# Optimization experiments

Measured on AMD Instinct MI355X. Metric: run time of the kernel, lower is better.

The kernel has to match this reference:

```python
import jax, jax.numpy as jnp
import numpy as np

# plan steps: (downsample_factor, bins_min, bins_max)
PLAN = [(2, 10, 14), (4, 16, 20)]


def _downsample(x, scale):
    # F.interpolate(mode='linear', align_corners=False, scale_factor=1/scale)
    in_len = x.shape[-1]
    out_len = in_len // scale
    sf = in_len / out_len
    src = jnp.maximum((jnp.arange(out_len, dtype=jnp.float32) + 0.5) * sf - 0.5, 0.0)
    i0 = jnp.floor(src).astype(jnp.int32)
    w = src - i0
    i1 = jnp.minimum(i0 + 1, in_len - 1)
    return x[..., i0] * (1.0 - w) + x[..., i1] * w


def _groupshiftadd(x, g):
    # one FFA butterfly stage with group size g
    B, C, R, nc = x.shape
    xg = x.reshape(B, C, R // g, g, nc)
    i = np.arange(g)
    iA = i // 2
    iB = iA + g // 2
    Bs = (i + 1) // 2
    # roll(v, Bs): y[j] = v[(j - Bs) mod nc]; static gather indices
    col = (np.arange(nc)[None, :] - Bs[:, None]) % nc  # (g, nc)
    a = xg[:, :, :, iA, :]                     # (B,C,G,g,nc)
    b = xg[:, :, :, iB[:, None], col]          # (B,C,G,g,nc) shifted rows
    return (a + b).reshape(B, C, R, nc)


def _forward(x):
    std_dev = jnp.std(x, axis=2, ddof=1)  # torch .std(2) is unbiased
    outs = []
    for ds, bmin, bmax in PLAN:
        down = _downsample(x, ds)
        L = down.shape[-1]
        for bins in range(bmin, bmax):
            trunc = L % bins
            arr = down[:, :, :L - trunc] if trunc else down
            r = arr.reshape(arr.shape[0], arr.shape[1], -1, bins)
            ini_rows = r.shape[2]
            k = int(np.ceil(np.log2(ini_rows)))
            target_rows = 2 ** k
            add = target_rows - ini_rows
            if add:
                pad = jnp.zeros((r.shape[0], r.shape[1], add, bins), r.dtype)
                r = jnp.concatenate([r, pad], axis=2)
            y = r
            for stage in range(1, k + 1):
                y = _groupshiftadd(y, 2 ** stage)
            mx = y.max(axis=3)
            # torch.median returns lower middle element for even sizes
            med = jnp.sort(y, axis=3)[..., (bins - 1) // 2]
            snr = (mx - med) / std_dev[:, :, None] / np.sqrt(float(ini_rows))
            outs.append(snr)  # (B, C, target_rows)
    return jnp.concatenate(outs, axis=2)


def setup_inputs() -> dict:
    key = jax.random.key(0)
    x = jax.random.normal(key, (8, 4, 262144), dtype=jnp.float32)
    return {"x": x}


def reference(x):
    return _forward(x)
```

## Files before the change

kernel.cpp:

```cpp
#include <hip/hip_runtime.h>
#include <cmath>


constexpr int NSEQ    = 32;
constexpr int NLEN    = 262144;
constexpr int OUTROWS = 81920;
constexpr int STDCH   = 32;

constexpr int cilog2(int v) { int r = 0; while (v > 1) { v >>= 1; ++r; } return r; }

constexpr size_t SCROFF[8] = {0, 6291456, 12582912, 18874368,
                              27262976, 29360128, 31981568, 34603008};

__device__ __forceinline__ unsigned bf16rne(float f) {
    unsigned u = __float_as_uint(f);
    return (u + 0x7FFFu + ((u >> 16) & 1u)) >> 16;
}
__device__ __forceinline__ unsigned pk2(float lo, float hi) {
    return bf16rne(lo) | (bf16rne(hi) << 16);
}
__device__ __forceinline__ int swz(int r) { return r ^ (((r >> 4) & 7) << 2); }

__device__ __forceinline__ void wfence()
{
    __builtin_amdgcn_sched_barrier(0);
    asm volatile("s_waitcnt lgkmcnt(0)" ::: "memory");
    __builtin_amdgcn_sched_barrier(0);
    __builtin_amdgcn_wave_barrier();
}

template<bool BAR>
__device__ __forceinline__ void stsync()
{
    if constexpr (BAR) __syncthreads();
    else wfence();
}

__global__ __launch_bounds__(256)
void std_partial(const float* __restrict__ x, float2* __restrict__ part)
{
    const int seq = blockIdx.x, ch = blockIdx.y;
    constexpr int N4 = NLEN / 4 / STDCH;
    const float4* xp = reinterpret_cast<const float4*>(x + (size_t)seq * NLEN) + (size_t)ch * N4;
    float s = 0.f, s2 = 0.f;
    for (int i = threadIdx.x; i < N4; i += 256) {
        float4 v = xp[i];
        s  += (v.x + v.y) + (v.z + v.w);
        s2 += (v.x * v.x + v.y * v.y) + (v.z * v.z + v.w * v.w);
    }
    #pragma unroll
    for (int off = 32; off > 0; off >>= 1) {
        s  += __shfl_down(s, off, 64);
        s2 += __shfl_down(s2, off, 64);
    }
    __shared__ float2 ws[4];
    const int w = threadIdx.x >> 6, l = threadIdx.x & 63;
    if (l == 0) ws[w] = make_float2(s, s2);
    __syncthreads();
    if (threadIdx.x == 0) {
        float a = ws[0].x + ws[1].x + ws[2].x + ws[3].x;
        float b = ws[0].y + ws[1].y + ws[2].y + ws[3].y;
        part[seq * STDCH + ch] = make_float2(a, b);
    }
}

template<int BINS, int G, int HB, bool BAR>
__device__ __forceinline__
void fusedA1ip(float* __restrict__ buf, int Q, int c0)
{
    constexpr int CST = G + 4;
    const int r4 = swz(4 * Q);
    float4 ff[HB + 3];
    #pragma unroll
    for (int j = 0; j < HB + 3; ++j) {
        int cc = c0 - 3 + j;
        if (cc < 0) cc += BINS;
        if (cc >= BINS) cc -= BINS;
        ff[j] = *reinterpret_cast<const float4*>(&buf[cc * CST + r4]);
    }
    stsync<BAR>();
    #pragma unroll
    for (int i = 0; i < HB; ++i) {
        const int c = c0 + i;
        if (c < BINS) {
            float4 f = ff[i + 3], fm1 = ff[i + 2], fm2 = ff[i + 1], fm3 = ff[i];
            float u0 = f.x + f.y;
            float u1 = f.x + fm1.y;
            float4 o;
            o.x = u0 + (f.z + f.w);
            o.y = u0 + (fm1.z + fm1.w);
            o.z = u1 + (fm1.z + fm2.w);
            o.w = u1 + (fm2.z + fm3.w);
            *reinterpret_cast<float4*>(&buf[c * CST + r4]) = o;
        }
    }
    stsync<BAR>();
}

template<int BINS, int G, int HB, bool BAR>
__device__ __forceinline__
void fusedAip(float* __restrict__ buf, int s, int Q, int c0)
{
    constexpr int CST = G + 4;
    const int h = 1 << (s - 1), S = 1 << s;
    const int q  = Q & (h - 1);
    const int G2 = (Q >> (s - 1)) << (s + 1);
    const int rA0 = swz(G2 + q),     rA1 = swz(G2 + q + h);
    const int rB0 = swz(G2 + S + q), rB1 = swz(G2 + S + q + h);
    const int vo  = swz(G2 + 4 * q);
    auto mbf = [](int x) { int r = x % BINS; return r < 0 ? r + BINS : r; };
    const int ba1 = mbf(c0 - q - 1);
    const int bb0 = mbf(c0 - 2 * q - 2);
    const int bb1 = mbf(c0 - 3 * q - 3);

    float fa0[HB], fa1[HB + 1], fb0[HB + 2], fb1[HB + 3];
    #pragma unroll
    for (int i = 0; i < HB; ++i) {
        int cc = c0 + i; if (cc >= BINS) cc = BINS - 1;
        fa0[i] = buf[cc * CST + rA0];
    }
    int idx = ba1;
    #pragma unroll
    for (int i = 0; i < HB + 1; ++i) {
        fa1[i] = buf[idx * CST + rA1];
        ++idx; if (idx == BINS) idx = 0;
    }
    idx = bb0;
    #pragma unroll
    for (int i = 0; i < HB + 2; ++i) {
        fb0[i] = buf[idx * CST + rB0];
        ++idx; if (idx == BINS) idx = 0;
    }
    idx = bb1;
    #pragma unroll
    for (int i = 0; i < HB + 3; ++i) {
        fb1[i] = buf[idx * CST + rB1];
        ++idx; if (idx == BINS) idx = 0;
    }
    stsync<BAR>();
    #pragma unroll
    for (int i = 0; i < HB; ++i) {
        const int c = c0 + i;
        if (c < BINS) {
            float u0 = fa0[i] + fa1[i + 1];
            float u1 = fa0[i] + fa1[i];
            float v0c  = fb0[i + 2] + fb1[i + 3];
            float v0p  = fb0[i + 1] + fb1[i + 2];
            float v1p  = fb0[i + 1] + fb1[i + 1];
            float v1pp = fb0[i]     + fb1[i];
            float4 o; o.x = u0 + v0c; o.y = u0 + v0p; o.z = u1 + v1p; o.w = u1 + v1pp;
            *reinterpret_cast<float4*>(&buf[c * CST + vo]) = o;
        }
    }
    stsync<BAR>();
}

template<int BINS, int G, int H1>
__device__ __forceinline__
void stage9IP(float* __restrict__ buf, int pr, int c0)
{
    constexpr int CST = G + 4;
    const int sA = swz(pr);
    const int sB = sA + 256;
    const int so = swz(2 * pr);
    const int shift = pr % BINS;

    float ra[H1], rb[H1 + 1];
    #pragma unroll
    for (int i = 0; i < H1; ++i) {
        int cc = c0 + i; if (cc >= BINS) cc = BINS - 1;
        ra[i] = buf[cc * CST + sA];
    }
    int idx = c0 - shift - 1;
    idx %= BINS; if (idx < 0) idx += BINS;
    #pragma unroll
    for (int i = 0; i < H1 + 1; ++i) {
        rb[i] = buf[idx * CST + sB];
        ++idx; if (idx == BINS) idx = 0;
    }
    __syncthreads();
    #pragma unroll
    for (int i = 0; i < H1; ++i) {
        const int c = c0 + i;
        if (c < BINS) {
            float2 o; o.x = ra[i] + rb[i + 1]; o.y = ra[i] + rb[i];
            *reinterpret_cast<float2*>(&buf[c * CST + so]) = o;
        }
    }
    __syncthreads();
}

template<int DS, int BINS, int K, int S0, int CPAD>
__device__ __forceinline__
void passA_body(float* __restrict__ buf, const float* __restrict__ xs,
                unsigned short* __restrict__ scrC, int R, int blk, int sl)
{
    constexpr int G     = 1 << S0;
    constexpr int M     = 1 << (K - S0);
    constexpr int CST   = G + 4;
    constexpr int QUADS = G / 4;
    constexpr int CHB   = 512 / QUADS;
    constexpr int LCHB  = cilog2(CHB);
    constexpr int QPW   = QUADS / 8;
    constexpr int HB    = (BINS + CHB - 1) / CHB;
    constexpr int CS1   = 512 / (G / 2);
    constexpr int H1    = (BINS + CS1 - 1) / CS1;
    const int t = threadIdx.x;

    const int fmax = max(0, min(G * BINS, R * BINS - blk * G * BINS));
    if (fmax <= 0) return;

    if constexpr (DS == 2) {
        const float4* src4 = reinterpret_cast<const float4*>(xs + 2 * (size_t)blk * G * BINS);
        constexpr int NF4 = G * BINS / 2;
        for (int i = t; i < NF4; i += 512) {
            const int f0 = 2 * i;
            if (f0 < fmax) {
                float4 v = src4[i];
                int lr = f0 / BINS, c = f0 - lr * BINS;
                buf[c * CST + swz(lr)] = 0.5f * (v.x + v.y);
                if (f0 + 1 < fmax) {
                    int c1 = c + 1, lr1 = lr;
                    if (c1 == BINS) { c1 = 0; ++lr1; }
                    buf[c1 * CST + swz(lr1)] = 0.5f * (v.z + v.w);
                }
            }
        }
    } else {
        const float4* src4 = reinterpret_cast<const float4*>(xs + 4 * (size_t)blk * G * BINS);
        constexpr int NF4 = G * BINS;
        for (int i = t; i < NF4; i += 512) {
            if (i < fmax) {
                float4 v = src4[i];
                int lr = i / BINS, c = i - lr * BINS;
                buf[c * CST + swz(lr)] = 0.5f * (v.y + v.z);
            }
        }
    }
    for (int f = fmax + t; f < G * BINS; f += 512) {
        int lr = f / BINS, c = f - lr * BINS;
        buf[c * CST + swz(lr)] = 0.f;
    }
    __syncthreads();

    {
        const int w = t >> 6, l = t & 63;
        const int Q  = w * QPW + (l >> LCHB);
        const int c0 = (l & (CHB - 1)) * HB;
        if constexpr (S0 == 9) {
            fusedA1ip<BINS, G, HB, false>(buf, Q, c0);
            fusedAip <BINS, G, HB, false>(buf, 3, Q, c0);
            fusedAip <BINS, G, HB, false>(buf, 5, Q, c0);
            __syncthreads();
            fusedAip <BINS, G, HB, true >(buf, 7, Q, c0);
        } else {
            fusedA1ip<BINS, G, HB, false>(buf, Q, c0);
            fusedAip <BINS, G, HB, false>(buf, 3, Q, c0);
            __syncthreads();
            fusedAip <BINS, G, HB, true >(buf, 5, Q, c0);
            fusedAip <BINS, G, HB, true >(buf, 7, Q, c0);
        }
    }
    if constexpr (S0 == 9) {
        const int pr  = t & (G / 2 - 1);
        const int c01 = (t >> (S0 - 1)) * H1;
        stage9IP<BINS, G, H1>(buf, pr, c01);
    }

    const float* fin = buf;
    if constexpr (G == 512) {
        const int lr = swz(t);
        unsigned u[CPAD / 2];
        #pragma unroll
        for (int k = 0; k < CPAD / 2; ++k) {
            const int ca = 2 * k, cbn = 2 * k + 1;
            float fa = (ca < BINS)  ? fin[ca * CST + lr]  : 0.f;
            float fb = (cbn < BINS) ? fin[cbn * CST + lr] : 0.f;
            u[k] = pk2(fa, fb);
        }
        unsigned short* dst = scrC + ((size_t)(sl * M + blk) * G + t) * CPAD;
        if constexpr (CPAD == 12) {
            uint2* d2 = reinterpret_cast<uint2*>(dst);
            d2[0] = make_uint2(u[0], u[1]);
            d2[1] = make_uint2(u[2], u[3]);
            d2[2] = make_uint2(u[4], u[5]);
        } else {
            uint4* d4 = reinterpret_cast<uint4*>(dst);
            d4[0] = make_uint4(u[0], u[1], u[2], u[3]);
            d4[1] = make_uint4(u[4], u[5], u[6], u[7]);
        }
    } else {
        const int lrn = t & 255, chh = t >> 8;
        const int lr = swz(lrn);
        constexpr int CH = CPAD / 2;
        unsigned u[CH / 2];
        #pragma unroll
        for (int k = 0; k < CH / 2; ++k) {
            const int ca = chh * CH + 2 * k, cbn = ca + 1;
            float fa = (ca < BINS)  ? fin[ca * CST + lr]  : 0.f;
            float fb = (cbn < BINS) ? fin[cbn * CST + lr] : 0.f;
            u[k] = pk2(fa, fb);
        }
        unsigned short* dst = scrC + ((size_t)(sl * M + blk) * G + lrn) * CPAD + chh * CH;
        if constexpr (CH == 8) {
            *reinterpret_cast<uint4*>(dst) = make_uint4(u[0], u[1], u[2], u[3]);
        } else {
            unsigned* d = reinterpret_cast<unsigned*>(dst);
            #pragma unroll
            for (int k = 0; k < CH / 2; ++k) d[k] = u[k];
        }
    }
}

__global__ __launch_bounds__(512, 6)
void passA_all(const float* __restrict__ x, unsigned short* __restrict__ scr)
{
    __shared__ float buf[13 * 516];
    const int b = blockIdx.x;
    if (b < 4096) {
        const int cfg = b >> 10, r = b & 1023, blk = r & 31, sl = r >> 5;
        const float* xs = x + (size_t)sl * NLEN;
        switch (cfg) {
            case 0: passA_body<2, 10, 14, 9, 12>(buf, xs, scr + SCROFF[0], 13107, blk, sl); break;
            case 1: passA_body<2, 11, 14, 9, 12>(buf, xs, scr + SCROFF[1], 11915, blk, sl); break;
            case 2: passA_body<2, 12, 14, 9, 12>(buf, xs, scr + SCROFF[2], 10922, blk, sl); break;
            default: passA_body<2, 13, 14, 9, 16>(buf, xs, scr + SCROFF[3], 10082, blk, sl); break;
        }
    } else {
        const int b2 = b - 4096;
        const int cfg = b2 >> 9, r = b2 & 511, blk = r & 15, sl = r >> 4;
        const float* xs = x + (size_t)sl * NLEN;
        switch (cfg) {
            case 0: passA_body<4, 16, 12, 8, 16>(buf, xs, scr + SCROFF[4], 4096, blk, sl); break;
            case 1: passA_body<4, 17, 12, 8, 20>(buf, xs, scr + SCROFF[5], 3855, blk, sl); break;
            case 2: passA_body<4, 18, 12, 8, 20>(buf, xs, scr + SCROFF[6], 3640, blk, sl); break;
            default: passA_body<4, 19, 12, 8, 20>(buf, xs, scr + SCROFF[7], 3449, blk, sl); break;
        }
    }
}

template<int BINS, int M, int CST, int HB, int LQ>
__device__ __forceinline__
void fusedB(float* __restrict__ zpg, int s, int p, int sub)
{
    constexpr int QUADS = M / 4;
    const int Q   = sub & (QUADS - 1);
    const int chi = sub >> LQ;
    const int c0  = chi * HB;
    const int h = 1 << (s - 1), S = 1 << s;
    const int q  = Q & (h - 1);
    const int G2 = (Q >> (s - 1)) << (s + 1);
    const int rA0 = G2 + q, rA1 = rA0 + h, rB0 = G2 + S + q, rB1 = rB0 + h;
    const int vo = G2 + 4 * q;
    auto mbf = [](int x, int B) { int r = x % B; return r < 0 ? r + B : r; };
    const int ba1 = mbf(c0 - q - p * h - 1, BINS);
    const int bb0 = mbf(c0 - 2 * q - p * S - 2, BINS);
    const int bb1 = mbf(c0 - 3 * q - p * (S + h) - 3, BINS);

    float fa0[HB], fa1[HB + 1], fb0[HB + 2], fb1[HB + 3];
    #pragma unroll
    for (int i = 0; i < HB; ++i) {
        int cc = c0 + i; if (cc >= BINS) cc = BINS - 1;
        fa0[i] = zpg[cc * CST + rA0];
    }
    int idx = ba1;
    #pragma unroll
    for (int i = 0; i < HB + 1; ++i) {
        fa1[i] = zpg[idx * CST + rA1];
        ++idx; if (idx == BINS) idx = 0;
    }
    idx = bb0;
    #pragma unroll
    for (int i = 0; i < HB + 2; ++i) {
        fb0[i] = zpg[idx * CST + rB0];
        ++idx; if (idx == BINS) idx = 0;
    }
    idx = bb1;
    #pragma unroll
    for (int i = 0; i < HB + 3; ++i) {
        fb1[i] = zpg[idx * CST + rB1];
        ++idx; if (idx == BINS) idx = 0;
    }
    __syncthreads();
    #pragma unroll
    for (int i2 = 0; i2 < HB; ++i2) {
        const int c = c0 + i2;
        if (c < BINS) {
            float u0 = fa0[i2] + fa1[i2 + 1];
            float u1 = fa0[i2] + fa1[i2];
            float v0c  = fb0[i2 + 2] + fb1[i2 + 3];
            float v0p  = fb0[i2 + 1] + fb1[i2 + 2];
            float v1p  = fb0[i2 + 1] + fb1[i2 + 1];
            float v1pp = fb0[i2]     + fb1[i2];
            float4 o; o.x = u0 + v0c; o.y = u0 + v0p; o.z = u1 + v1p; o.w = u1 + v1pp;
            *reinterpret_cast<float4*>(&zpg[c * CST + vo]) = o;
        }
    }
    __syncthreads();
}

template<int BINS, int M, int CST, int HSB, int LP>
__device__ __forceinline__
void singleB(float* __restrict__ zpg, int s, int p, int sub)
{
    constexpr int PAIRSB = M / 2;
    const int pr  = sub & (PAIRSB - 1);
    const int chi = sub >> LP;
    const int c0  = chi * HSB;
    const int half = 1 << (s - 1);
    const int qp = pr & (half - 1);
    const int grpbase = (pr >> (s - 1)) << s;
    const int rA = grpbase + qp, rB = rA + half, ro = grpbase + 2 * qp;
    const int shift = (qp + p * half) % BINS;

    float ra[HSB], rb[HSB + 1];
    #pragma unroll
    for (int i = 0; i < HSB; ++i) {
        int cc = c0 + i; if (cc >= BINS) cc = BINS - 1;
        ra[i] = zpg[cc * CST + rA];
    }
    int idx = c0 - shift - 1;
    idx %= BINS; if (idx < 0) idx += BINS;
    #pragma unroll
    for (int i = 0; i < HSB + 1; ++i) {
        rb[i] = zpg[idx * CST + rB];
        ++idx; if (idx == BINS) idx = 0;
    }
    __syncthreads();
    #pragma unroll
    for (int i2 = 0; i2 < HSB; ++i2) {
        const int c = c0 + i2;
        if (c < BINS) {
            float2 o; o.x = ra[i2] + rb[i2 + 1]; o.y = ra[i2] + rb[i2];
            *reinterpret_cast<float2*>(&zpg[c * CST + ro]) = o;
        }
    }
    __syncthreads();
}

template<int BINS, int K, int S0, int CPAD, int OUTOFF>
__device__ __forceinline__
void passB_body(float* __restrict__ zb, float* __restrict__ s_red,
                const unsigned short* __restrict__ scrC, const float2* __restrict__ part,
                float* __restrict__ out, int R, int p_base, int sl)
{
    constexpr int G    = 1 << S0;
    constexpr int M    = 1 << (K - S0);
    constexpr int TS   = K - S0;
    constexpr int P    = 16;
    constexpr int CST  = M + 4;
    constexpr int BCST = BINS * CST;
    constexpr int LQB  = cilog2(M / 4);
    constexpr int CHB  = 32 / (M / 4);
    constexpr int HB   = (BINS + CHB - 1) / CHB;
    constexpr int LPB  = cilog2(M / 2);
    constexpr int CSB  = 32 / (M / 2);
    constexpr int HSB  = (BINS + CSB - 1) / CSB;

    const int t = threadIdx.x;

    if (t < 64) {
        float s = 0.f, s2 = 0.f;
        if (t < 32) { float2 pp = part[sl * STDCH + t]; s = pp.x; s2 = pp.y; }
        #pragma unroll
        for (int off = 16; off > 0; off >>= 1) {
            s  += __shfl_down(s, off, 64);
            s2 += __shfl_down(s2, off, 64);
        }
        if (t == 0) {
            const float n = (float)NLEN;
            s_red[0] = rsqrtf((s2 - s * s / n) / (n - 1.f)) * rsqrtf((float)R);
        }
    }

    {
        constexpr int RUN = P * CPAD / 4;
        constexpr int TOT = M * RUN;
        const int vmax = (R + G - 1) >> S0;
        const unsigned short* base = scrC + (size_t)sl * M * G * CPAD + (size_t)p_base * CPAD;
        for (int i = t; i < TOT; i += 512) {
            const int v = i / RUN, r = i - v * RUN;
            uint2 d = make_uint2(0u, 0u);
            if (v < vmax)
                d = *reinterpret_cast<const uint2*>(base + (size_t)v * G * CPAD + 4 * r);
            const int e0 = 4 * r;
            const int pl = e0 / CPAD, c = e0 - pl * CPAD;
            float* zp = zb + pl * BCST + v;
            if (c + 0 < BINS) zp[(c + 0) * CST] = __uint_as_float(d.x << 16);
            if (c + 1 < BINS) zp[(c + 1) * CST] = __uint_as_float(d.x & 0xFFFF0000u);
            if (c + 2 < BINS) zp[(c + 2) * CST] = __uint_as_float(d.y << 16);
            if (c + 3 < BINS) zp[(c + 3) * CST] = __uint_as_float(d.y & 0xFFFF0000u);
        }
    }
    __syncthreads();

    const int sub = t & 31, pg = t >> 5;
    const int p = p_base + pg;
    float* zpg = zb + pg * BCST;
    fusedB<BINS, M, CST, HB, LQB>(zpg, 1, p, sub);
    fusedB<BINS, M, CST, HB, LQB>(zpg, 3, p, sub);
    if constexpr (TS == 5) {
        singleB<BINS, M, CST, HSB, LPB>(zpg, 5, p, sub);
    }

    constexpr int ROWS = P * M;
    if (t < ROWS) {
        const int pg2 = t >> TS;
        const int v   = t & (M - 1);
        const float* z = zb + pg2 * BCST;
        float a[BINS];
        #pragma unroll
        for (int c = 0; c < BINS; ++c) a[c] = z[c * CST + v];
        float mx = a[0];
        #pragma unroll
        for (int c = 1; c < BINS; ++c) mx = fmaxf(mx, a[c]);
        constexpr int MIDX = (BINS - 1) / 2;
        #pragma unroll
        for (int i = 0; i <= MIDX; ++i) {
            #pragma unroll
            for (int j = i + 1; j < BINS; ++j) {
                float lo = fminf(a[i], a[j]);
                float hi = fmaxf(a[i], a[j]);
                a[i] = lo; a[j] = hi;
            }
        }
        out[(size_t)sl * OUTROWS + OUTOFF + (size_t)p_base * M + t] = (mx - a[MIDX]) * s_red[0];
    }
}

__global__ __launch_bounds__(512, 6)
void passB_all(const unsigned short* __restrict__ scr, const float2* __restrict__ part,
               float* __restrict__ out)
{
    __shared__ float zb[16 * 13 * 36];
    __shared__ float s_red[1];
    const int b = blockIdx.x;
    if (b < 4096) {
        const int cfg = b >> 10, r = b & 1023, pb = r & 31, sl = r >> 5;
        const int p_base = pb * 16;
        switch (cfg) {
            case 0: passB_body<10, 14, 9, 12, 0>    (zb, s_red, scr + SCROFF[0], part, out, 13107, p_base, sl); break;
            case 1: passB_body<11, 14, 9, 12, 16384>(zb, s_red, scr + SCROFF[1], part, out, 11915, p_base, sl); break;
            case 2: passB_body<12, 14, 9, 12, 32768>(zb, s_red, scr + SCROFF[2], part, out, 10922, p_base, sl); break;
            default: passB_body<13, 14, 9, 16, 49152>(zb, s_red, scr + SCROFF[3], part, out, 10082, p_base, sl); break;
        }
    } else {
        const int b2 = b - 4096;
        const int cfg = b2 >> 9, r = b2 & 511, pb = r & 15, sl = r >> 4;
        const int p_base = pb * 16;
        switch (cfg) {
            case 0: passB_body<16, 12, 8, 16, 65536>(zb, s_red, scr + SCROFF[4], part, out, 4096, p_base, sl); break;
            case 1: passB_body<17, 12, 8, 20, 69632>(zb, s_red, scr + SCROFF[5], part, out, 3855, p_base, sl); break;
            case 2: passB_body<18, 12, 8, 20, 73728>(zb, s_red, scr + SCROFF[6], part, out, 3640, p_base, sl); break;
            default: passB_body<19, 12, 8, 20, 77824>(zb, s_red, scr + SCROFF[7], part, out, 3449, p_base, sl); break;
        }
    }
}

extern "C" void kernel_launch(void* const* d_in, const int* in_sizes, int n_in,
                              void* d_out, int out_size, void* d_ws, size_t ws_size,
                              hipStream_t stream)
{
    (void)in_sizes; (void)n_in; (void)out_size; (void)ws_size;
    const float* x = (const float*)d_in[0];
    float* out  = (float*)d_out;
    float* wsf  = (float*)d_ws;
    float2* part = reinterpret_cast<float2*>(wsf + 64);
    unsigned short* scr = reinterpret_cast<unsigned short*>(wsf + 2176);

    hipLaunchKernelGGL(std_partial, dim3(NSEQ, STDCH), dim3(256), 0, stream, x, part);
    hipLaunchKernelGGL(passA_all, dim3(6144), dim3(512), 0, stream, x, scr);
    hipLaunchKernelGGL(passB_all, dim3(6144), dim3(512), 0, stream, scr, part, out);
}
```

Measured before the change: 144.7 us.

## Split FFA stages as 8+6 for ds=2 configs, use 256-thread passA blocks

Pass A now always handles a 256-row group (8 butterfly stages) with 256-thread blocks, so the ds=2 configurations launch twice as many smaller blocks and no longer need the separate stage-9 in-place step with its extra barriers. Pass B in turn takes over the sixth stage for those configurations, processing 8 periods per block with 64 threads each and running three fused stage pairs. This trades a larger pass-B working set and different LDS footprints for smaller pass-A blocks, higher occupancy and fewer block-wide syncs.

Measured after the change: 142.2 us (median of 2 runs). Within noise of the previous version (-1.8%).

```diff
diff --git a/kernel.cpp b/kernel.cpp
--- a/kernel.cpp
+++ b/kernel.cpp
@@ -28,7 +28,6 @@
     __builtin_amdgcn_sched_barrier(0);
     __builtin_amdgcn_wave_barrier();
 }
-
 template<bool BAR>
 __device__ __forceinline__ void stsync()
 {
@@ -155,56 +154,20 @@
     stsync<BAR>();
 }
 
-template<int BINS, int G, int H1>
-__device__ __forceinline__
-void stage9IP(float* __restrict__ buf, int pr, int c0)
-{
-    constexpr int CST = G + 4;
-    const int sA = swz(pr);
-    const int sB = sA + 256;
-    const int so = swz(2 * pr);
-    const int shift = pr % BINS;
-
-    float ra[H1], rb[H1 + 1];
-    #pragma unroll
-    for (int i = 0; i < H1; ++i) {
-        int cc = c0 + i; if (cc >= BINS) cc = BINS - 1;
-        ra[i] = buf[cc * CST + sA];
-    }
-    int idx = c0 - shift - 1;
-    idx %= BINS; if (idx < 0) idx += BINS;
-    #pragma unroll
-    for (int i = 0; i < H1 + 1; ++i) {
-        rb[i] = buf[idx * CST + sB];
-        ++idx; if (idx == BINS) idx = 0;
-    }
-    __syncthreads();
-    #pragma unroll
-    for (int i = 0; i < H1; ++i) {
-        const int c = c0 + i;
-        if (c < BINS) {
-            float2 o; o.x = ra[i] + rb[i + 1]; o.y = ra[i] + rb[i];
-            *reinterpret_cast<float2*>(&buf[c * CST + so]) = o;
-        }
-    }
-    __syncthreads();
-}
-
-template<int DS, int BINS, int K, int S0, int CPAD>
+template<int DS, int BINS, int K, int CPAD>
 __device__ __forceinline__
 void passA_body(float* __restrict__ buf, const float* __restrict__ xs,
                 unsigned short* __restrict__ scrC, int R, int blk, int sl)
 {
-    constexpr int G     = 1 << S0;
+    constexpr int S0    = 8;
+    constexpr int G     = 256;
     constexpr int M     = 1 << (K - S0);
     constexpr int CST   = G + 4;
     constexpr int QUADS = G / 4;
-    constexpr int CHB   = 512 / QUADS;
-    constexpr int LCHB  = cilog2(CHB);
-    constexpr int QPW   = QUADS / 8;
+    constexpr int CHB   = 4;
+    constexpr int LCHB  = 2;
+    constexpr int QPW   = QUADS / 4;
     constexpr int HB    = (BINS + CHB - 1) / CHB;
-    constexpr int CS1   = 512 / (G / 2);
-    constexpr int H1    = (BINS + CS1 - 1) / CS1;
     const int t = threadIdx.x;
 
     const int fmax = max(0, min(G * BINS, R * BINS - blk * G * BINS));
@@ -213,7 +176,7 @@
     if constexpr (DS == 2) {
         const float4* src4 = reinterpret_cast<const float4*>(xs + 2 * (size_t)blk * G * BINS);
         constexpr int NF4 = G * BINS / 2;
-        for (int i = t; i < NF4; i += 512) {
+        for (int i = t; i < NF4; i += 256) {
             const int f0 = 2 * i;
             if (f0 < fmax) {
                 float4 v = src4[i];
@@ -229,7 +192,7 @@
     } else {
         const float4* src4 = reinterpret_cast<const float4*>(xs + 4 * (size_t)blk * G * BINS);
         constexpr int NF4 = G * BINS;
-        for (int i = t; i < NF4; i += 512) {
+        for (int i = t; i < NF4; i += 256) {
             if (i < fmax) {
                 float4 v = src4[i];
                 int lr = i / BINS, c = i - lr * BINS;
@@ -237,7 +200,7 @@
             }
         }
     }
-    for (int f = fmax + t; f < G * BINS; f += 512) {
+    for (int f = fmax + t; f < G * BINS; f += 256) {
         int lr = f / BINS, c = f - lr * BINS;
         buf[c * CST + swz(lr)] = 0.f;
     }
@@ -247,94 +210,60 @@
         const int w = t >> 6, l = t & 63;
         const int Q  = w * QPW + (l >> LCHB);
         const int c0 = (l & (CHB - 1)) * HB;
-        if constexpr (S0 == 9) {
-            fusedA1ip<BINS, G, HB, false>(buf, Q, c0);
-            fusedAip <BINS, G, HB, false>(buf, 3, Q, c0);
-            fusedAip <BINS, G, HB, false>(buf, 5, Q, c0);
-            __syncthreads();
-            fusedAip <BINS, G, HB, true >(buf, 7, Q, c0);
-        } else {
-            fusedA1ip<BINS, G, HB, false>(buf, Q, c0);
-            fusedAip <BINS, G, HB, false>(buf, 3, Q, c0);
-            __syncthreads();
-            fusedAip <BINS, G, HB, true >(buf, 5, Q, c0);
-            fusedAip <BINS, G, HB, true >(buf, 7, Q, c0);
-        }
-    }
-    if constexpr (S0 == 9) {
-        const int pr  = t & (G / 2 - 1);
-        const int c01 = (t >> (S0 - 1)) * H1;
-        stage9IP<BINS, G, H1>(buf, pr, c01);
-    }
-
-    const float* fin = buf;
-    if constexpr (G == 512) {
+        fusedA1ip<BINS, G, HB, false>(buf, Q, c0);
+        fusedAip <BINS, G, HB, false>(buf, 3, Q, c0);
+        fusedAip <BINS, G, HB, false>(buf, 5, Q, c0);
+        __syncthreads();
+        fusedAip <BINS, G, HB, true >(buf, 7, Q, c0);
+    }
+
+    {
         const int lr = swz(t);
         unsigned u[CPAD / 2];
         #pragma unroll
         for (int k = 0; k < CPAD / 2; ++k) {
             const int ca = 2 * k, cbn = 2 * k + 1;
-            float fa = (ca < BINS)  ? fin[ca * CST + lr]  : 0.f;
-            float fb = (cbn < BINS) ? fin[cbn * CST + lr] : 0.f;
+            float fa = (ca < BINS)  ? buf[ca * CST + lr]  : 0.f;
+            float fb = (cbn < BINS) ? buf[cbn * CST + lr] : 0.f;
             u[k] = pk2(fa, fb);
         }
         unsigned short* dst = scrC + ((size_t)(sl * M + blk) * G + t) * CPAD;
-        if constexpr (CPAD == 12) {
-            uint2* d2 = reinterpret_cast<uint2*>(dst);
-            d2[0] = make_uint2(u[0], u[1]);
-            d2[1] = make_uint2(u[2], u[3]);
-            d2[2] = make_uint2(u[4], u[5]);
-        } else {
+        if constexpr (CPAD == 16) {
             uint4* d4 = reinterpret_cast<uint4*>(dst);
             d4[0] = make_uint4(u[0], u[1], u[2], u[3]);
             d4[1] = make_uint4(u[4], u[5], u[6], u[7]);
-        }
-    } else {
-        const int lrn = t & 255, chh = t >> 8;
-        const int lr = swz(lrn);
-        constexpr int CH = CPAD / 2;
-        unsigned u[CH / 2];
-        #pragma unroll
-        for (int k = 0; k < CH / 2; ++k) {
-            const int ca = chh * CH + 2 * k, cbn = ca + 1;
-            float fa = (ca < BINS)  ? fin[ca * CST + lr]  : 0.f;
-            float fb = (cbn < BINS) ? fin[cbn * CST + lr] : 0.f;
-            u[k] = pk2(fa, fb);
-        }
-        unsigned short* dst = scrC + ((size_t)(sl * M + blk) * G + lrn) * CPAD + chh * CH;
-        if constexpr (CH == 8) {
-            *reinterpret_cast<uint4*>(dst) = make_uint4(u[0], u[1], u[2], u[3]);
         } else {
-            unsigned* d = reinterpret_cast<unsigned*>(dst);
+            uint2* d2 = reinterpret_cast<uint2*>(dst);
             #pragma unroll
-            for (int k = 0; k < CH / 2; ++k) d[k] = u[k];
-        }
-    }
-}
-
-__global__ __launch_bounds__(512, 6)
+            for (int k = 0; k < CPAD / 4; ++k)
+                d2[k] = make_uint2(u[2 * k], u[2 * k + 1]);
+        }
+    }
+}
+
+__global__ __launch_bounds__(256, 8)
 void passA_all(const float* __restrict__ x, unsigned short* __restrict__ scr)
 {
-    __shared__ float buf[13 * 516];
+    __shared__ float buf[19 * 260];
     const int b = blockIdx.x;
-    if (b < 4096) {
-        const int cfg = b >> 10, r = b & 1023, blk = r & 31, sl = r >> 5;
+    if (b < 8192) {
+        const int cfg = b >> 11, r = b & 2047, blk = r & 63, sl = r >> 6;
         const float* xs = x + (size_t)sl * NLEN;
         switch (cfg) {
-            case 0: passA_body<2, 10, 14, 9, 12>(buf, xs, scr + SCROFF[0], 13107, blk, sl); break;
-            case 1: passA_body<2, 11, 14, 9, 12>(buf, xs, scr + SCROFF[1], 11915, blk, sl); break;
-            case 2: passA_body<2, 12, 14, 9, 12>(buf, xs, scr + SCROFF[2], 10922, blk, sl); break;
-            default: passA_body<2, 13, 14, 9, 16>(buf, xs, scr + SCROFF[3], 10082, blk, sl); break;
+            case 0: passA_body<2, 10, 14, 12>(buf, xs, scr + SCROFF[0], 13107, blk, sl); break;
+            case 1: passA_body<2, 11, 14, 12>(buf, xs, scr + SCROFF[1], 11915, blk, sl); break;
+            case 2: passA_body<2, 12, 14, 12>(buf, xs, scr + SCROFF[2], 10922, blk, sl); break;
+            default: passA_body<2, 13, 14, 16>(buf, xs, scr + SCROFF[3], 10082, blk, sl); break;
         }
     } else {
-        const int b2 = b - 4096;
+        const int b2 = b - 8192;
         const int cfg = b2 >> 9, r = b2 & 511, blk = r & 15, sl = r >> 4;
         const float* xs = x + (size_t)sl * NLEN;
         switch (cfg) {
-            case 0: passA_body<4, 16, 12, 8, 16>(buf, xs, scr + SCROFF[4], 4096, blk, sl); break;
-            case 1: passA_body<4, 17, 12, 8, 20>(buf, xs, scr + SCROFF[5], 3855, blk, sl); break;
-            case 2: passA_body<4, 18, 12, 8, 20>(buf, xs, scr + SCROFF[6], 3640, blk, sl); break;
-            default: passA_body<4, 19, 12, 8, 20>(buf, xs, scr + SCROFF[7], 3449, blk, sl); break;
+            case 0: passA_body<4, 16, 12, 16>(buf, xs, scr + SCROFF[4], 4096, blk, sl); break;
+            case 1: passA_body<4, 17, 12, 20>(buf, xs, scr + SCROFF[5], 3855, blk, sl); break;
+            case 2: passA_body<4, 18, 12, 20>(buf, xs, scr + SCROFF[6], 3640, blk, sl); break;
+            default: passA_body<4, 19, 12, 20>(buf, xs, scr + SCROFF[7], 3449, blk, sl); break;
         }
     }
 }
@@ -399,63 +328,23 @@
     __syncthreads();
 }
 
-template<int BINS, int M, int CST, int HSB, int LP>
-__device__ __forceinline__
-void singleB(float* __restrict__ zpg, int s, int p, int sub)
-{
-    constexpr int PAIRSB = M / 2;
-    const int pr  = sub & (PAIRSB - 1);
-    const int chi = sub >> LP;
-    const int c0  = chi * HSB;
-    const int half = 1 << (s - 1);
-    const int qp = pr & (half - 1);
-    const int grpbase = (pr >> (s - 1)) << s;
-    const int rA = grpbase + qp, rB = rA + half, ro = grpbase + 2 * qp;
-    const int shift = (qp + p * half) % BINS;
-
-    float ra[HSB], rb[HSB + 1];
-    #pragma unroll
-    for (int i = 0; i < HSB; ++i) {
-        int cc = c0 + i; if (cc >= BINS) cc = BINS - 1;
-        ra[i] = zpg[cc * CST + rA];
-    }
-    int idx = c0 - shift - 1;
-    idx %= BINS; if (idx < 0) idx += BINS;
-    #pragma unroll
-    for (int i = 0; i < HSB + 1; ++i) {
-        rb[i] = zpg[idx * CST + rB];
-        ++idx; if (idx == BINS) idx = 0;
-    }
-    __syncthreads();
-    #pragma unroll
-    for (int i2 = 0; i2 < HSB; ++i2) {
-        const int c = c0 + i2;
-        if (c < BINS) {
-            float2 o; o.x = ra[i2] + rb[i2 + 1]; o.y = ra[i2] + rb[i2];
-            *reinterpret_cast<float2*>(&zpg[c * CST + ro]) = o;
-        }
-    }
-    __syncthreads();
-}
-
-template<int BINS, int K, int S0, int CPAD, int OUTOFF>
+template<int BINS, int K, int P, int CPAD, int OUTOFF>
 __device__ __forceinline__
 void passB_body(float* __restrict__ zb, float* __restrict__ s_red,
                 const unsigned short* __restrict__ scrC, const float2* __restrict__ part,
                 float* __restrict__ out, int R, int p_base, int sl)
 {
-    constexpr int G    = 1 << S0;
+    constexpr int S0   = 8;
+    constexpr int G    = 256;
     constexpr int M    = 1 << (K - S0);
     constexpr int TS   = K - S0;
-    constexpr int P    = 16;
     constexpr int CST  = M + 4;
     constexpr int BCST = BINS * CST;
+    constexpr int SUBW = 512 / P;
+    constexpr int LSUB = cilog2(SUBW);
     constexpr int LQB  = cilog2(M / 4);
-    constexpr int CHB  = 32 / (M / 4);
+    constexpr int CHB  = SUBW / (M / 4);
     constexpr int HB   = (BINS + CHB - 1) / CHB;
-    constexpr int LPB  = cilog2(M / 2);
-    constexpr int CSB  = 32 / (M / 2);
-    constexpr int HSB  = (BINS + CSB - 1) / CSB;
 
     const int t = threadIdx.x;
 
@@ -494,14 +383,12 @@
     }
     __syncthreads();
 
-    const int sub = t & 31, pg = t >> 5;
+    const int sub = t & (SUBW - 1), pg = t >> LSUB;
     const int p = p_base + pg;
     float* zpg = zb + pg * BCST;
-    fusedB<BINS, M, CST, HB, LQB>(zpg, 1, p, sub);
-    fusedB<BINS, M, CST, HB, LQB>(zpg, 3, p, sub);
-    if constexpr (TS == 5) {
-        singleB<BINS, M, CST, HSB, LPB>(zpg, 5, p, sub);
-    }
+    #pragma unroll
+    for (int s = 1; s <= TS; s += 2)
+        fusedB<BINS, M, CST, HB, LQB>(zpg, s, p, sub);
 
     constexpr int ROWS = P * M;
     if (t < ROWS) {
@@ -532,27 +419,27 @@
 void passB_all(const unsigned short* __restrict__ scr, const float2* __restrict__ part,
                float* __restrict__ out)
 {
-    __shared__ float zb[16 * 13 * 36];
+    __shared__ float zb[8 * 13 * 68];
     __shared__ float s_red[1];
     const int b = blockIdx.x;
     if (b < 4096) {
         const int cfg = b >> 10, r = b & 1023, pb = r & 31, sl = r >> 5;
-        const int p_base = pb * 16;
+        const int p_base = pb * 8;
         switch (cfg) {
-            case 0: passB_body<10, 14, 9, 12, 0>    (zb, s_red, scr + SCROFF[0], part, out, 13107, p_base, sl); break;
-            case 1: passB_body<11, 14, 9, 12, 16384>(zb, s_red, scr + SCROFF[1], part, out, 11915, p_base, sl); break;
-            case 2: passB_body<12, 14, 9, 12, 32768>(zb, s_red, scr + SCROFF[2], part, out, 10922, p_base, sl); break;
-            default: passB_body<13, 14, 9, 16, 49152>(zb, s_red, scr + SCROFF[3], part, out, 10082, p_base, sl); break;
+            case 0: passB_body<10, 14, 8, 12, 0>    (zb, s_red, scr + SCROFF[0], part, out, 13107, p_base, sl); break;
+            case 1: passB_body<11, 14, 8, 12, 16384>(zb, s_red, scr + SCROFF[1], part, out, 11915, p_base, sl); break;
+            case 2: passB_body<12, 14, 8, 12, 32768>(zb, s_red, scr + SCROFF[2], part, out, 10922, p_base, sl); break;
+            default: passB_body<13, 14, 8, 16, 49152>(zb, s_red, scr + SCROFF[3], part, out, 10082, p_base, sl); break;
         }
     } else {
         const int b2 = b - 4096;
         const int cfg = b2 >> 9, r = b2 & 511, pb = r & 15, sl = r >> 4;
         const int p_base = pb * 16;
         switch (cfg) {
-            case 0: passB_body<16, 12, 8, 16, 65536>(zb, s_red, scr + SCROFF[4], part, out, 4096, p_base, sl); break;
-            case 1: passB_body<17, 12, 8, 20, 69632>(zb, s_red, scr + SCROFF[5], part, out, 3855, p_base, sl); break;
-            case 2: passB_body<18, 12, 8, 20, 73728>(zb, s_red, scr + SCROFF[6], part, out, 3640, p_base, sl); break;
-            default: passB_body<19, 12, 8, 20, 77824>(zb, s_red, scr + SCROFF[7], part, out, 3449, p_base, sl); break;
+            case 0: passB_body<16, 12, 16, 16, 65536>(zb, s_red, scr + SCROFF[4], part, out, 4096, p_base, sl); break;
+            case 1: passB_body<17, 12, 16, 20, 69632>(zb, s_red, scr + SCROFF[5], part, out, 3855, p_base, sl); break;
+            case 2: passB_body<18, 12, 16, 20, 73728>(zb, s_red, scr + SCROFF[6], part, out, 3640, p_base, sl); break;
+            default: passB_body<19, 12, 16, 20, 77824>(zb, s_red, scr + SCROFF[7], part, out, 3449, p_base, sl); break;
         }
     }
 }
@@ -569,6 +456,6 @@
     unsigned short* scr = reinterpret_cast<unsigned short*>(wsf + 2176);
 
     hipLaunchKernelGGL(std_partial, dim3(NSEQ, STDCH), dim3(256), 0, stream, x, part);
-    hipLaunchKernelGGL(passA_all, dim3(6144), dim3(512), 0, stream, x, scr);
+    hipLaunchKernelGGL(passA_all, dim3(10240), dim3(256), 0, stream, x, scr);
     hipLaunchKernelGGL(passB_all, dim3(6144), dim3(512), 0, stream, scr, part, out);
 }
```
